# Kernel tuning notes

Measured on AMD Instinct MI355X. Metric: run time of the kernel, lower is better.

Reference implementation:

```python
import jax, jax.numpy as jnp
import numpy as np

B, L, HID = 2, 2048, 1024
H, D = 16, 64            # num_attention_heads, attention_head_size
R = 512                  # projection_rank = basis_rank
MAX_ORDER = 5
NUM_BASIS = MAX_ORDER + 1  # min(basis_rank, max_order+1)
TOPK = 64


def _orthogonal_basis(seq_len, num_basis, dtype=jnp.float32):
    # Orthonormal DCT-II basis evaluated at relative distance d=|i-j|.
    # basis[i, j, k] = s_k * cos(pi * (d + 0.5) * k / L), s_0=sqrt(1/L), s_k=sqrt(2/L)
    idx = jnp.arange(seq_len)
    d = jnp.abs(idx[:, None] - idx[None, :]).astype(dtype)          # [L, L]
    k = jnp.arange(num_basis, dtype=dtype)                          # [K]
    basis = jnp.cos(jnp.pi * (d[..., None] + 0.5) * k / seq_len)    # [L, L, K]
    scale = jnp.where(k == 0, jnp.sqrt(1.0 / seq_len), jnp.sqrt(2.0 / seq_len))
    return basis * scale


def _topk_mask(seq_len, topk):
    # keep top-k nearest neighbors by |i-j| per row (stable argsort tie-break)
    idx = jnp.arange(seq_len)
    dist = jnp.abs(idx[:, None] - idx[None, :])
    k = min(topk, seq_len)
    cols = jnp.argsort(dist, axis=-1)[:, :k]                        # [L, k]
    rows = jnp.broadcast_to(idx[:, None], (seq_len, k))
    mask = jnp.zeros((seq_len, seq_len), dtype=bool).at[rows, cols].set(True)
    return mask


def setup_inputs() -> dict:
    key = jax.random.key(0)
    ks = jax.random.split(key, 10)
    s = 0.02
    inp = {
        "hidden_states": jax.random.normal(ks[0], (B, L, HID), jnp.float32),
        "Wq": jax.random.normal(ks[1], (HID, HID), jnp.float32) * s,
        "bq": jnp.zeros((HID,), jnp.float32),
        "Wk": jax.random.normal(ks[2], (HID, HID), jnp.float32) * s,
        "bk": jnp.zeros((HID,), jnp.float32),
        "Wv": jax.random.normal(ks[3], (HID, HID), jnp.float32) * s,
        "bv": jnp.zeros((HID,), jnp.float32),
        "coefficients": jax.random.normal(ks[4], (H, NUM_BASIS), jnp.float32) * s,
    }
    # orthogonal-ish init for the low-rank projections [H, D, R]
    def ortho(k):
        m = jax.random.normal(k, (H * D, R), jnp.float32)
        q, _ = jnp.linalg.qr(m)
        return q.reshape(H, D, R)
    inp["q_proj_weight"] = ortho(ks[5])
    inp["k_proj_weight"] = ortho(ks[6])
    return inp


def reference(hidden_states, Wq, bq, Wk, bk, Wv, bv, coefficients,
              q_proj_weight, k_proj_weight):
    bsz, tgt_len, _ = hidden_states.shape

    def shape(x):  # [B, L, HID] -> [B, H, L, D]
        return x.reshape(bsz, tgt_len, H, D).transpose(0, 2, 1, 3)

    q = shape(hidden_states @ Wq + bq)
    k = shape(hidden_states @ Wk + bk)
    v = shape(hidden_states @ Wv + bv)

    qp = jnp.einsum('bhld,hdr->bhlr', q, q_proj_weight)
    kp = jnp.einsum('bhld,hdr->bhlr', k, k_proj_weight)
    scores = jnp.einsum('bhlr,bhmr->bhlm', qp, kp) / jnp.sqrt(jnp.float32(R))

    basis = _orthogonal_basis(tgt_len, NUM_BASIS, scores.dtype)      # [L, L, K]
    bias = jnp.einsum('hk,ijk->hij', coefficients, basis)            # [H, L, L]
    bias = bias * _topk_mask(tgt_len, TOPK)[None, :, :]
    scores = scores + bias[None]

    probs = jax.nn.softmax(scores, axis=-1)                          # dropout: eval mode
    ctx = jnp.einsum('bhlm,bhmd->bhld', probs, v)
    return ctx.transpose(0, 2, 1, 3).reshape(bsz, tgt_len, H * D)
```

## Files before the change

kernel.cpp:

```cpp
#include <hip/hip_runtime.h>

typedef short bf16x8 __attribute__((ext_vector_type(8)));
typedef float f32x4 __attribute__((ext_vector_type(4)));

#define L_SEQ 2048

__device__ inline unsigned short f2bf(float f) {
    unsigned int u = __builtin_bit_cast(unsigned int, f);
    u += 0x7FFFu + ((u >> 16) & 1u);
    return (unsigned short)(u >> 16);
}

__device__ inline float exp2_fast(float x) {
    float r;
    asm volatile("v_exp_f32 %0, %1" : "=v"(r) : "v"(x));
    return r;
}

__device__ inline void gload16(const void* g, void* l) {
    __builtin_amdgcn_global_load_lds((const __attribute__((address_space(1))) void*)g,
                                     (__attribute__((address_space(3))) void*)l, 16, 0, 0);
}

__global__ __launch_bounds__(256) void compute_M(const float* __restrict__ Pq,
                                                 const float* __restrict__ Pk,
                                                 float* __restrict__ M) {
    const int h = blockIdx.x, dg = blockIdx.y, t = threadIdx.x;
    const int e = t & 63, dr = t >> 6;
    __shared__ float Pql[4][512];
    for (int i = t; i < 512; i += 256) {
#pragma unroll
        for (int rr = 0; rr < 4; ++rr)
            Pql[rr][i] = Pq[((size_t)h * 64 + dg * 4 + rr) * 512 + i];
    }
    __syncthreads();
    const float4* a = (const float4*)Pql[dr];
    const float4* b = (const float4*)(Pk + ((size_t)h * 64 + e) * 512);
    float s = 0.f;
#pragma unroll 4
    for (int r = 0; r < 128; ++r) {
        float4 x = a[r], y = b[r];
        s = fmaf(x.x, y.x, fmaf(x.y, y.y, fmaf(x.z, y.z, fmaf(x.w, y.w, s))));
    }
    M[((size_t)h * 64 + dg * 4 + dr) * 64 + e] =
        s * (0.044194173824159216f * 1.4426950408889634f);
}

__global__ void bias_table_kernel(const float* __restrict__ coef, float* __restrict__ fbias) {
    int i = blockIdx.x * 256 + threadIdx.x;
    if (i >= 16 * 2048) return;
    int h = i >> 11, d = i & 2047;
    const float pi = 3.14159265358979323846f;
    float acc = 0.f;
#pragma unroll
    for (int k = 0; k < 6; ++k) {
        float sc = (k == 0) ? 0.022097086912079608f : 0.03125f;
        float arg = pi * ((float)d + 0.5f) * (float)k * (1.0f / 2048.0f);
        acc += coef[h * 6 + k] * sc * cosf(arg);
    }
    fbias[i] = acc * 1.4426950408889634f;
}

__global__ __launch_bounds__(256) void build_wtq(
    const float* __restrict__ Wq, const float* __restrict__ bq, const float* __restrict__ M,
    unsigned short* __restrict__ Wt, float* __restrict__ biasp) {
    const int hh = blockIdx.x, kt = blockIdx.y, t = threadIdx.x;
    const int k0 = kt * 64;
    __shared__ float Wql[64 * 68];
    __shared__ float MlT[64 * 65];

    for (int i = t; i < 4096; i += 256) {
        int d = i >> 6, e = i & 63;
        MlT[e * 65 + d] = M[(size_t)hh * 4096 + i];
    }
#pragma unroll
    for (int i = 0; i < 4; ++i) {
        int cc = i * 256 + t;
        int row = cc >> 4, c4 = cc & 15;
        *(float4*)&Wql[row * 68 + c4 * 4] =
            *(const float4*)(Wq + (size_t)(k0 + row) * 1024 + hh * 64 + c4 * 4);
    }
    __syncthreads();

    const int e = t >> 2, kq = t & 3;
    float me[64];
#pragma unroll
    for (int d = 0; d < 64; ++d) me[d] = MlT[e * 65 + d];

    float acc[16];
#pragma unroll
    for (int i = 0; i < 16; ++i) acc[i] = 0.f;
#pragma unroll
    for (int kk = 0; kk < 16; ++kk) {
        int row = kq * 16 + kk;
#pragma unroll
        for (int d4 = 0; d4 < 16; ++d4) {
            float4 w = *(const float4*)&Wql[row * 68 + d4 * 4];
            acc[kk] = fmaf(w.x, me[d4 * 4 + 0],
                      fmaf(w.y, me[d4 * 4 + 1],
                      fmaf(w.z, me[d4 * 4 + 2],
                      fmaf(w.w, me[d4 * 4 + 3], acc[kk]))));
        }
    }
    unsigned short* dp = Wt + (size_t)(hh * 64 + e) * 1024 + k0 + kq * 16;
#pragma unroll
    for (int q8 = 0; q8 < 2; ++q8) {
        unsigned short o8[8];
#pragma unroll
        for (int j = 0; j < 8; ++j) o8[j] = f2bf(acc[q8 * 8 + j]);
        *(uint4*)(dp + q8 * 8) = *(const uint4*)o8;
    }
    if (kt == 0 && t < 64) {
        float s = 0.f;
#pragma unroll
        for (int d = 0; d < 64; ++d) s = fmaf(bq[hh * 64 + d], MlT[t * 65 + d], s);
        biasp[hh * 64 + t] = s;
    }
}

__global__ __launch_bounds__(256) void transpose_wkv(
    const float* __restrict__ Wk, const float* __restrict__ Wv,
    const float* __restrict__ bk, const float* __restrict__ bv,
    unsigned short* __restrict__ Wt, float* __restrict__ biasp) {
    const int ct = blockIdx.x, kt2 = blockIdx.y, sel = blockIdx.z;
    const float* W = sel ? Wv : Wk;
    __shared__ float tl[64 * 68];
    const int t = threadIdx.x;
    const int k0 = kt2 * 64, c0 = ct * 64;
#pragma unroll
    for (int i = 0; i < 4; ++i) {
        int cc = i * 256 + t;
        int r = cc >> 4, c4 = cc & 15;
        *(float4*)&tl[r * 68 + c4 * 4] =
            *(const float4*)(W + (size_t)(k0 + r) * 1024 + c0 + c4 * 4);
    }
    __syncthreads();
    const int c = t >> 2, seg = t & 3;
    unsigned short* dp = Wt + (size_t)(1024 + sel * 1024 + c0 + c) * 1024 + k0 + seg * 16;
#pragma unroll
    for (int q8 = 0; q8 < 2; ++q8) {
        unsigned short o8[8];
#pragma unroll
        for (int j = 0; j < 8; ++j) o8[j] = f2bf(tl[(seg * 16 + q8 * 8 + j) * 68 + c]);
        *(uint4*)(dp + q8 * 8) = *(const uint4*)o8;
    }
    if (kt2 == 0 && t < 64) biasp[1024 + sel * 1024 + c0 + t] = (sel ? bv : bk)[c0 + t];
}

__global__ __launch_bounds__(256) void cast_hs_kernel(const float* __restrict__ hs,
                                                      unsigned short* __restrict__ X) {
    const int i = (blockIdx.x * 256 + threadIdx.x) * 4;
    float4 v = *(const float4*)(hs + i);
    unsigned short o[4] = {f2bf(v.x), f2bf(v.y), f2bf(v.z), f2bf(v.w)};
    *(uint2*)(X + i) = *(const uint2*)o;
}

__global__ __launch_bounds__(512) void gemm_qkv(
    const unsigned short* __restrict__ X, const unsigned short* __restrict__ Wt,
    const float* __restrict__ biasp,
    unsigned short* __restrict__ qs, unsigned short* __restrict__ ksd,
    unsigned short* __restrict__ vt) {
    __shared__ __align__(16) unsigned short shm[4 * 8192];

    const int bn = blockIdx.x, bm = blockIdx.y;
    const int m0 = bm * 128, n0 = bn * 128;
    const int t = threadIdx.x, wave = t >> 6, lane = t & 63, g = lane >> 4, li = lane & 15;
    const int wr = wave >> 2, wc = wave & 3;

    const int rowb = t >> 3;
    const int soff = ((t & 7) ^ (rowb & 7)) * 8;
    const unsigned short* Xrow = X + (size_t)(m0 + rowb) * 1024 + soff;
    const unsigned short* Wrow = Wt + (size_t)(n0 + rowb) * 1024 + soff;

    f32x4 acc[4][2];
#pragma unroll
    for (int i = 0; i < 4; ++i)
#pragma unroll
        for (int j = 0; j < 2; ++j) acc[i][j] = (f32x4){0.f, 0.f, 0.f, 0.f};

#pragma unroll
    for (int i = 0; i < 2; ++i) {
        gload16(Xrow + (size_t)i * 64 * 1024, &shm[(i * 512 + t) * 8]);
        gload16(Wrow + (size_t)i * 64 * 1024, &shm[16384 + (i * 512 + t) * 8]);
    }

    for (int kt = 0; kt < 16; ++kt) {
        const int cur = kt & 1;
        __builtin_amdgcn_s_barrier();
        if (kt < 15) {
            const int k0n = (kt + 1) * 64;
            unsigned short* An = &shm[(cur ^ 1) * 8192];
            unsigned short* Bn = &shm[16384 + (cur ^ 1) * 8192];
#pragma unroll
            for (int i = 0; i < 2; ++i) {
                gload16(Xrow + (size_t)i * 64 * 1024 + k0n, &An[(i * 512 + t) * 8]);
                gload16(Wrow + (size_t)i * 64 * 1024 + k0n, &Bn[(i * 512 + t) * 8]);
            }
            asm volatile("s_waitcnt vmcnt(4)" ::: "memory");
        } else {
            asm volatile("s_waitcnt vmcnt(0)" ::: "memory");
        }
        __builtin_amdgcn_s_barrier();
        const unsigned short* Al = &shm[cur * 8192];
        const unsigned short* Bl = &shm[16384 + cur * 8192];
        __builtin_amdgcn_s_setprio(1);
#pragma unroll
        for (int ks = 0; ks < 2; ++ks) {
            bf16x8 af[4], bf[2];
#pragma unroll
            for (int mi = 0; mi < 4; ++mi) {
                int row = wr * 64 + mi * 16 + li;
                af[mi] = *(const bf16x8*)&Al[row * 64 + ((ks * 4 + g) ^ (row & 7)) * 8];
            }
#pragma unroll
            for (int ni = 0; ni < 2; ++ni) {
                int row = wc * 32 + ni * 16 + li;
                bf[ni] = *(const bf16x8*)&Bl[row * 64 + ((ks * 4 + g) ^ (row & 7)) * 8];
            }
#pragma unroll
            for (int mi = 0; mi < 4; ++mi)
#pragma unroll
                for (int ni = 0; ni < 2; ++ni)
                    acc[mi][ni] = __builtin_amdgcn_mfma_f32_16x16x32_bf16(af[mi], bf[ni],
                                                                          acc[mi][ni], 0, 0, 0);
        }
        __builtin_amdgcn_s_setprio(0);
    }
    __syncthreads();

    float bvals[2];
#pragma unroll
    for (int ni = 0; ni < 2; ++ni) bvals[ni] = biasp[n0 + wc * 32 + ni * 16 + li];

    const int region = n0 >> 10;
    float* scr = (float*)shm;

    if (region < 2) {
        float* wf = scr + wave * (16 * 36);
        unsigned short* dstbase = region == 0 ? qs : ksd;
        const int ncol0 = n0 + wc * 32;
        const int hh = (ncol0 & 1023) >> 6;
        const int dcol = (ncol0 & 63) + (lane & 3) * 8;
        const int lr = lane >> 2;
#pragma unroll
        for (int mi = 0; mi < 4; ++mi) {
#pragma unroll
            for (int r = 0; r < 4; ++r) {
                int rowl = g * 4 + r;
#pragma unroll
                for (int ni = 0; ni < 2; ++ni)
                    wf[rowl * 36 + ni * 16 + li] = acc[mi][ni][r] + bvals[ni];
            }
            int m = m0 + wr * 64 + mi * 16 + lr;
            int bb = m >> 11, l = m & 2047;
            unsigned short* dp = dstbase + ((size_t)(bb * 16 + hh) * 2048 + l) * 64 + dcol;
            float4 a0 = *(const float4*)&wf[lr * 36 + (lane & 3) * 8];
            float4 a1 = *(const float4*)&wf[lr * 36 + (lane & 3) * 8 + 4];
            unsigned short o8[8] = {f2bf(a0.x), f2bf(a0.y), f2bf(a0.z), f2bf(a0.w),
                                    f2bf(a1.x), f2bf(a1.y), f2bf(a1.z), f2bf(a1.w)};
            *(uint4*)dp = *(const uint4*)o8;
        }
    } else {
        float* wf = scr + wave * (32 * 36);
        const int d32 = lane & 31, half = lane >> 5;
        const int dglob = ((n0 + wc * 32) & 63) + d32;
        const int hh = ((n0 + wc * 32) & 1023) >> 6;
#pragma unroll
        for (int ch2 = 0; ch2 < 2; ++ch2) {
#pragma unroll
            for (int mi2 = 0; mi2 < 2; ++mi2) {
                int mi = ch2 * 2 + mi2;
#pragma unroll
                for (int r = 0; r < 4; ++r) {
                    int rowl = mi2 * 16 + g * 4 + r;
#pragma unroll
                    for (int ni = 0; ni < 2; ++ni)
                        wf[rowl * 36 + ni * 16 + li] = acc[mi][ni][r] + bvals[ni];
                }
            }
            int l0 = m0 + wr * 64 + ch2 * 32;
            int bb = l0 >> 11, lb = (l0 & 2047) + half * 16;
            unsigned short* dp = vt + ((size_t)(bb * 16 + hh) * 64 + dglob) * 2048 + lb;
#pragma unroll
            for (int q8 = 0; q8 < 2; ++q8) {
                unsigned short o8[8];
#pragma unroll
                for (int j = 0; j < 8; ++j)
                    o8[j] = f2bf(wf[(half * 16 + q8 * 8 + j) * 36 + d32]);
                *(uint4*)(dp + q8 * 8) = *(const uint4*)o8;
            }
        }
    }
}

__global__ __launch_bounds__(512) void attn_kernel(
    const unsigned short* __restrict__ qs, const unsigned short* __restrict__ ksrc,
    const unsigned short* __restrict__ vt, const float* __restrict__ fbias,
    float* __restrict__ out) {
    const int qt = blockIdx.x, bh = blockIdx.y;
    const int h = bh & 15, b = bh >> 4;
    const int t = threadIdx.x, wave = t >> 6, lane = t & 63, g = lane >> 4, li = lane & 15;

    __shared__ unsigned short Klds[2][2][64 * 64];
    __shared__ unsigned short Vlds[2][2][64 * 64];
    __shared__ unsigned short Plds[8][16 * 64];

    const float* fbh = fbias + (size_t)h * 2048;
    const unsigned short* Kg = ksrc + (size_t)bh * L_SEQ * 64;
    const unsigned short* Vg = vt + (size_t)bh * 64 * L_SEQ;

    const int im = qt * 128 + wave * 16;
    const unsigned short* qb = qs + ((size_t)bh * L_SEQ + im + li) * 64;
    bf16x8 qa0 = *(const bf16x8*)(qb + g * 8);
    bf16x8 qa1 = *(const bf16x8*)(qb + 32 + g * 8);

    bf16x8 onesv;
#pragma unroll
    for (int i = 0; i < 8; ++i) onesv[i] = (short)0x3F80;

    f32x4 o[5];
#pragma unroll
    for (int i = 0; i < 5; ++i) o[i] = (f32x4){0.f, 0.f, 0.f, 0.f};

    const int iout0 = im + g * 4;

    int lo_min = im - 32; lo_min = lo_min < 0 ? 0 : (lo_min > 1984 ? 1984 : lo_min);
    int hi_tmp = im + 15 - 32; hi_tmp = hi_tmp < 0 ? 0 : (hi_tmp > 1984 ? 1984 : hi_tmp);
    const int hi_max = hi_tmp + 63;

    const int r0 = t >> 3, s0 = ((t & 7) ^ (r0 & 7)) * 8;

#pragma unroll
    for (int sub = 0; sub < 2; ++sub) {
        gload16(Kg + (size_t)(sub * 64 + r0) * 64 + s0, &Klds[0][sub][t * 8]);
        gload16(Vg + (size_t)r0 * L_SEQ + sub * 64 + s0, &Vlds[0][sub][t * 8]);
    }

    for (int jp = 0; jp < 16; ++jp) {
        const int cur = jp & 1;

        __builtin_amdgcn_s_barrier();
        if (jp < 15) {
            const int jb = (jp + 1) * 128;
#pragma unroll
            for (int sub = 0; sub < 2; ++sub) {
                gload16(Kg + (size_t)(jb + sub * 64 + r0) * 64 + s0, &Klds[cur ^ 1][sub][t * 8]);
                gload16(Vg + (size_t)r0 * L_SEQ + jb + sub * 64 + s0, &Vlds[cur ^ 1][sub][t * 8]);
            }
            asm volatile("s_waitcnt vmcnt(4)" ::: "memory");
        } else {
            asm volatile("s_waitcnt vmcnt(0)" ::: "memory");
        }
        __builtin_amdgcn_s_barrier();

#pragma unroll
        for (int sub = 0; sub < 2; ++sub) {
            const int j0 = jp * 128 + sub * 64;
            const unsigned short* Kl = Klds[cur][sub];
            const unsigned short* Vl = Vlds[cur][sub];

            f32x4 s[4];
#pragma unroll
            for (int nb = 0; nb < 4; ++nb) s[nb] = (f32x4){0.f, 0.f, 0.f, 0.f};
            __builtin_amdgcn_s_setprio(1);
#pragma unroll
            for (int ks = 0; ks < 2; ++ks) {
                bf16x8 qf = ks ? qa1 : qa0;
#pragma unroll
                for (int nb = 0; nb < 4; ++nb) {
                    int row = nb * 16 + li;
                    bf16x8 kf = *(const bf16x8*)&Kl[row * 64 + ((ks * 4 + g) ^ (row & 7)) * 8];
                    s[nb] = __builtin_amdgcn_mfma_f32_16x16x32_bf16(qf, kf, s[nb], 0, 0, 0);
                }
            }
            __builtin_amdgcn_s_setprio(0);

            const bool bias_tile = (j0 + 63 >= lo_min) && (j0 <= hi_max);
            unsigned short* Pw = Plds[wave];
#pragma unroll
            for (int r = 0; r < 4; ++r) {
                int iout = iout0 + r;
                int row = g * 4 + r;
                if (bias_tile) {
                    int lo = iout - 32;
                    lo = lo < 0 ? 0 : (lo > 1984 ? 1984 : lo);
#pragma unroll
                    for (int nb = 0; nb < 4; ++nb) {
                        int j = j0 + nb * 16 + li;
                        float x = s[nb][r];
                        int dd = iout - j; dd = dd < 0 ? -dd : dd;
                        if ((unsigned)(j - lo) < 64u) x += fbh[dd];
                        int col = nb * 16 + li;
                        Pw[row * 64 + (col ^ ((row & 7) << 3))] = f2bf(exp2_fast(x));
                    }
                } else {
#pragma unroll
                    for (int nb = 0; nb < 4; ++nb) {
                        int col = nb * 16 + li;
                        Pw[row * 64 + (col ^ ((row & 7) << 3))] = f2bf(exp2_fast(s[nb][r]));
                    }
                }
            }

            bf16x8 pa0 = *(const bf16x8*)&Pw[li * 64 + ((0 + g) ^ (li & 7)) * 8];
            bf16x8 pa1 = *(const bf16x8*)&Pw[li * 64 + ((4 + g) ^ (li & 7)) * 8];
            __builtin_amdgcn_s_setprio(1);
#pragma unroll
            for (int db = 0; db < 4; ++db) {
                int row = db * 16 + li;
                bf16x8 v0 = *(const bf16x8*)&Vl[row * 64 + ((0 + g) ^ (row & 7)) * 8];
                bf16x8 v1 = *(const bf16x8*)&Vl[row * 64 + ((4 + g) ^ (row & 7)) * 8];
                o[db] = __builtin_amdgcn_mfma_f32_16x16x32_bf16(pa0, v0, o[db], 0, 0, 0);
                o[db] = __builtin_amdgcn_mfma_f32_16x16x32_bf16(pa1, v1, o[db], 0, 0, 0);
            }
            o[4] = __builtin_amdgcn_mfma_f32_16x16x32_bf16(pa0, onesv, o[4], 0, 0, 0);
            o[4] = __builtin_amdgcn_mfma_f32_16x16x32_bf16(pa1, onesv, o[4], 0, 0, 0);
            __builtin_amdgcn_s_setprio(0);
        }
    }

    float* ob = out + (size_t)b * L_SEQ * 1024 + h * 64;
#pragma unroll
    for (int r = 0; r < 4; ++r) {
        float rl = 1.f / o[4][r];
        int iout = iout0 + r;
#pragma unroll
        for (int db = 0; db < 4; ++db)
            ob[(size_t)iout * 1024 + db * 16 + li] = o[db][r] * rl;
    }
}

extern "C" void kernel_launch(void* const* d_in, const int* in_sizes, int n_in,
                              void* d_out, int out_size, void* d_ws, size_t ws_size,
                              hipStream_t stream) {
    const float* hs = (const float*)d_in[0];
    const float* Wq = (const float*)d_in[1];
    const float* bq = (const float*)d_in[2];
    const float* Wk = (const float*)d_in[3];
    const float* bk = (const float*)d_in[4];
    const float* Wv = (const float*)d_in[5];
    const float* bv = (const float*)d_in[6];
    const float* coef = (const float*)d_in[7];
    const float* Pq = (const float*)d_in[8];
    const float* Pk = (const float*)d_in[9];
    float* out = (float*)d_out;

    char* w = (char*)d_ws;
    float* M = (float*)(w);
    float* fbias = (float*)(w + 0x40000);
    float* biasp = (float*)(w + 0x60000);
    unsigned short* Wt = (unsigned short*)(w + 0x70000);
    unsigned short* X = (unsigned short*)(w + 0x670000);
    unsigned short* qs = (unsigned short*)(w + 0xE70000);
    unsigned short* ks = (unsigned short*)(w + 0x1670000);
    unsigned short* vt = (unsigned short*)(w + 0x2670000);

    hipLaunchKernelGGL(compute_M, dim3(16, 16), dim3(256), 0, stream, Pq, Pk, M);
    hipLaunchKernelGGL(bias_table_kernel, dim3(128), dim3(256), 0, stream, coef, fbias);
    hipLaunchKernelGGL(build_wtq, dim3(16, 16), dim3(256), 0, stream, Wq, bq, M, Wt, biasp);
    hipLaunchKernelGGL(transpose_wkv, dim3(16, 16, 2), dim3(256), 0, stream,
                       Wk, Wv, bk, bv, Wt, biasp);
    hipLaunchKernelGGL(cast_hs_kernel, dim3(4096), dim3(256), 0, stream, hs, X);
    hipLaunchKernelGGL(gemm_qkv, dim3(24, 32), dim3(512), 0, stream, X, Wt, biasp, qs, ks, vt);
    hipLaunchKernelGGL(attn_kernel, dim3(16, 32), dim3(512), 0, stream, qs, ks, vt, fbias, out);
}
```

Before: 124.2 us.

## Process two 16-row query tiles per wave to reuse K/V fragments

```diff
diff --git a/kernel.cpp b/kernel.cpp
--- a/kernel.cpp
+++ b/kernel.cpp
@@ -303,29 +303,35 @@
 
     __shared__ unsigned short Klds[2][2][64 * 64];
     __shared__ unsigned short Vlds[2][2][64 * 64];
-    __shared__ unsigned short Plds[8][16 * 64];
+    __shared__ unsigned short Plds[8][32 * 64];
 
     const float* fbh = fbias + (size_t)h * 2048;
     const unsigned short* Kg = ksrc + (size_t)bh * L_SEQ * 64;
     const unsigned short* Vg = vt + (size_t)bh * 64 * L_SEQ;
 
-    const int im = qt * 128 + wave * 16;
+    const int im = qt * 256 + wave * 32;
     const unsigned short* qb = qs + ((size_t)bh * L_SEQ + im + li) * 64;
-    bf16x8 qa0 = *(const bf16x8*)(qb + g * 8);
-    bf16x8 qa1 = *(const bf16x8*)(qb + 32 + g * 8);
+    bf16x8 qa00 = *(const bf16x8*)(qb + g * 8);
+    bf16x8 qa01 = *(const bf16x8*)(qb + 32 + g * 8);
+    bf16x8 qa10 = *(const bf16x8*)(qb + 16 * 64 + g * 8);
+    bf16x8 qa11 = *(const bf16x8*)(qb + 16 * 64 + 32 + g * 8);
 
     bf16x8 onesv;
 #pragma unroll
     for (int i = 0; i < 8; ++i) onesv[i] = (short)0x3F80;
 
-    f32x4 o[5];
-#pragma unroll
-    for (int i = 0; i < 5; ++i) o[i] = (f32x4){0.f, 0.f, 0.f, 0.f};
-
-    const int iout0 = im + g * 4;
+    f32x4 oA[5], oB[5];
+#pragma unroll
+    for (int i = 0; i < 5; ++i) {
+        oA[i] = (f32x4){0.f, 0.f, 0.f, 0.f};
+        oB[i] = (f32x4){0.f, 0.f, 0.f, 0.f};
+    }
+
+    const int ioutA = im + g * 4;
+    const int ioutB = im + 16 + g * 4;
 
     int lo_min = im - 32; lo_min = lo_min < 0 ? 0 : (lo_min > 1984 ? 1984 : lo_min);
-    int hi_tmp = im + 15 - 32; hi_tmp = hi_tmp < 0 ? 0 : (hi_tmp > 1984 ? 1984 : hi_tmp);
+    int hi_tmp = im + 31 - 32; hi_tmp = hi_tmp < 0 ? 0 : (hi_tmp > 1984 ? 1984 : hi_tmp);
     const int hi_max = hi_tmp + 63;
 
     const int r0 = t >> 3, s0 = ((t & 7) ^ (r0 & 7)) * 8;
@@ -359,27 +365,39 @@
             const unsigned short* Kl = Klds[cur][sub];
             const unsigned short* Vl = Vlds[cur][sub];
 
-            f32x4 s[4];
-#pragma unroll
-            for (int nb = 0; nb < 4; ++nb) s[nb] = (f32x4){0.f, 0.f, 0.f, 0.f};
+            bf16x8 kf0[4], kf1[4];
+#pragma unroll
+            for (int nb = 0; nb < 4; ++nb) {
+                int row = nb * 16 + li;
+                kf0[nb] = *(const bf16x8*)&Kl[row * 64 + ((0 + g) ^ (row & 7)) * 8];
+                kf1[nb] = *(const bf16x8*)&Kl[row * 64 + ((4 + g) ^ (row & 7)) * 8];
+            }
+
+            f32x4 sA[4], sB[4];
+#pragma unroll
+            for (int nb = 0; nb < 4; ++nb) {
+                sA[nb] = (f32x4){0.f, 0.f, 0.f, 0.f};
+                sB[nb] = (f32x4){0.f, 0.f, 0.f, 0.f};
+            }
             __builtin_amdgcn_s_setprio(1);
 #pragma unroll
-            for (int ks = 0; ks < 2; ++ks) {
-                bf16x8 qf = ks ? qa1 : qa0;
-#pragma unroll
-                for (int nb = 0; nb < 4; ++nb) {
-                    int row = nb * 16 + li;
-                    bf16x8 kf = *(const bf16x8*)&Kl[row * 64 + ((ks * 4 + g) ^ (row & 7)) * 8];
-                    s[nb] = __builtin_amdgcn_mfma_f32_16x16x32_bf16(qf, kf, s[nb], 0, 0, 0);
-                }
+            for (int nb = 0; nb < 4; ++nb) {
+                sA[nb] = __builtin_amdgcn_mfma_f32_16x16x32_bf16(qa00, kf0[nb], sA[nb], 0, 0, 0);
+                sA[nb] = __builtin_amdgcn_mfma_f32_16x16x32_bf16(qa01, kf1[nb], sA[nb], 0, 0, 0);
+            }
+#pragma unroll
+            for (int nb = 0; nb < 4; ++nb) {
+                sB[nb] = __builtin_amdgcn_mfma_f32_16x16x32_bf16(qa10, kf0[nb], sB[nb], 0, 0, 0);
+                sB[nb] = __builtin_amdgcn_mfma_f32_16x16x32_bf16(qa11, kf1[nb], sB[nb], 0, 0, 0);
             }
             __builtin_amdgcn_s_setprio(0);
 
             const bool bias_tile = (j0 + 63 >= lo_min) && (j0 <= hi_max);
             unsigned short* Pw = Plds[wave];
+
 #pragma unroll
             for (int r = 0; r < 4; ++r) {
-                int iout = iout0 + r;
+                int iout = ioutA + r;
                 int row = g * 4 + r;
                 if (bias_tile) {
                     int lo = iout - 32;
@@ -387,7 +405,7 @@
 #pragma unroll
                     for (int nb = 0; nb < 4; ++nb) {
                         int j = j0 + nb * 16 + li;
-                        float x = s[nb][r];
+                        float x = sA[nb][r];
                         int dd = iout - j; dd = dd < 0 ? -dd : dd;
                         if ((unsigned)(j - lo) < 64u) x += fbh[dd];
                         int col = nb * 16 + li;
@@ -397,24 +415,63 @@
 #pragma unroll
                     for (int nb = 0; nb < 4; ++nb) {
                         int col = nb * 16 + li;
-                        Pw[row * 64 + (col ^ ((row & 7) << 3))] = f2bf(exp2_fast(s[nb][r]));
+                        Pw[row * 64 + (col ^ ((row & 7) << 3))] = f2bf(exp2_fast(sA[nb][r]));
                     }
                 }
             }
-
-            bf16x8 pa0 = *(const bf16x8*)&Pw[li * 64 + ((0 + g) ^ (li & 7)) * 8];
-            bf16x8 pa1 = *(const bf16x8*)&Pw[li * 64 + ((4 + g) ^ (li & 7)) * 8];
-            __builtin_amdgcn_s_setprio(1);
+#pragma unroll
+            for (int r = 0; r < 4; ++r) {
+                int iout = ioutB + r;
+                int row = 16 + g * 4 + r;
+                if (bias_tile) {
+                    int lo = iout - 32;
+                    lo = lo < 0 ? 0 : (lo > 1984 ? 1984 : lo);
+#pragma unroll
+                    for (int nb = 0; nb < 4; ++nb) {
+                        int j = j0 + nb * 16 + li;
+                        float x = sB[nb][r];
+                        int dd = iout - j; dd = dd < 0 ? -dd : dd;
+                        if ((unsigned)(j - lo) < 64u) x += fbh[dd];
+                        int col = nb * 16 + li;
+                        Pw[row * 64 + (col ^ ((row & 7) << 3))] = f2bf(exp2_fast(x));
+                    }
+                } else {
+#pragma unroll
+                    for (int nb = 0; nb < 4; ++nb) {
+                        int col = nb * 16 + li;
+                        Pw[row * 64 + (col ^ ((row & 7) << 3))] = f2bf(exp2_fast(sB[nb][r]));
+                    }
+                }
+            }
+
+            bf16x8 paA0 = *(const bf16x8*)&Pw[li * 64 + ((0 + g) ^ (li & 7)) * 8];
+            bf16x8 paA1 = *(const bf16x8*)&Pw[li * 64 + ((4 + g) ^ (li & 7)) * 8];
+            bf16x8 paB0 = *(const bf16x8*)&Pw[(16 + li) * 64 + ((0 + g) ^ ((16 + li) & 7)) * 8];
+            bf16x8 paB1 = *(const bf16x8*)&Pw[(16 + li) * 64 + ((4 + g) ^ ((16 + li) & 7)) * 8];
+
+            bf16x8 vf0[4], vf1[4];
 #pragma unroll
             for (int db = 0; db < 4; ++db) {
                 int row = db * 16 + li;
-                bf16x8 v0 = *(const bf16x8*)&Vl[row * 64 + ((0 + g) ^ (row & 7)) * 8];
-                bf16x8 v1 = *(const bf16x8*)&Vl[row * 64 + ((4 + g) ^ (row & 7)) * 8];
-                o[db] = __builtin_amdgcn_mfma_f32_16x16x32_bf16(pa0, v0, o[db], 0, 0, 0);
-                o[db] = __builtin_amdgcn_mfma_f32_16x16x32_bf16(pa1, v1, o[db], 0, 0, 0);
-            }
-            o[4] = __builtin_amdgcn_mfma_f32_16x16x32_bf16(pa0, onesv, o[4], 0, 0, 0);
-            o[4] = __builtin_amdgcn_mfma_f32_16x16x32_bf16(pa1, onesv, o[4], 0, 0, 0);
+                vf0[db] = *(const bf16x8*)&Vl[row * 64 + ((0 + g) ^ (row & 7)) * 8];
+                vf1[db] = *(const bf16x8*)&Vl[row * 64 + ((4 + g) ^ (row & 7)) * 8];
+            }
+
+            __builtin_amdgcn_s_setprio(1);
+#pragma unroll
+            for (int db = 0; db < 4; ++db) {
+                oA[db] = __builtin_amdgcn_mfma_f32_16x16x32_bf16(paA0, vf0[db], oA[db], 0, 0, 0);
+                oA[db] = __builtin_amdgcn_mfma_f32_16x16x32_bf16(paA1, vf1[db], oA[db], 0, 0, 0);
+            }
+            oA[4] = __builtin_amdgcn_mfma_f32_16x16x32_bf16(paA0, onesv, oA[4], 0, 0, 0);
+            oA[4] = __builtin_amdgcn_mfma_f32_16x16x32_bf16(paA1, onesv, oA[4], 0, 0, 0);
+#pragma unroll
+            for (int db = 0; db < 4; ++db) {
+                oB[db] = __builtin_amdgcn_mfma_f32_16x16x32_bf16(paB0, vf0[db], oB[db], 0, 0, 0);
+                oB[db] = __builtin_amdgcn_mfma_f32_16x16x32_bf16(paB1, vf1[db], oB[db], 0, 0, 0);
+            }
+            oB[4] = __builtin_amdgcn_mfma_f32_16x16x32_bf16(paB0, onesv, oB[4], 0, 0, 0);
+            oB[4] = __builtin_amdgcn_mfma_f32_16x16x32_bf16(paB1, onesv, oB[4], 0, 0, 0);
             __builtin_amdgcn_s_setprio(0);
         }
     }
@@ -422,11 +479,14 @@
     float* ob = out + (size_t)b * L_SEQ * 1024 + h * 64;
 #pragma unroll
     for (int r = 0; r < 4; ++r) {
-        float rl = 1.f / o[4][r];
-        int iout = iout0 + r;
-#pragma unroll
-        for (int db = 0; db < 4; ++db)
-            ob[(size_t)iout * 1024 + db * 16 + li] = o[db][r] * rl;
+        float rlA = 1.f / oA[4][r];
+        float rlB = 1.f / oB[4][r];
+        int ia = ioutA + r, ib = ioutB + r;
+#pragma unroll
+        for (int db = 0; db < 4; ++db) {
+            ob[(size_t)ia * 1024 + db * 16 + li] = oA[db][r] * rlA;
+            ob[(size_t)ib * 1024 + db * 16 + li] = oB[db][r] * rlB;
+        }
     }
 }
 
@@ -462,5 +522,5 @@
                        Wk, Wv, bk, bv, Wt, biasp);
     hipLaunchKernelGGL(cast_hs_kernel, dim3(4096), dim3(256), 0, stream, hs, X);
     hipLaunchKernelGGL(gemm_qkv, dim3(24, 32), dim3(512), 0, stream, X, Wt, biasp, qs, ks, vt);
-    hipLaunchKernelGGL(attn_kernel, dim3(16, 32), dim3(512), 0, stream, qs, ks, vt, fbias, out);
-}
+    hipLaunchKernelGGL(attn_kernel, dim3(8, 32), dim3(512), 0, stream, qs, ks, vt, fbias, out);
+}
```

Measured after the change: 137.7 us. 10.9% more time.

## Transpose MFMA operands in attention loop and compute softmax denominator via shuffles

Applied to the files above, without the earlier changes.

```diff
diff --git a/kernel.cpp b/kernel.cpp
--- a/kernel.cpp
+++ b/kernel.cpp
@@ -314,19 +314,19 @@
     bf16x8 qa0 = *(const bf16x8*)(qb + g * 8);
     bf16x8 qa1 = *(const bf16x8*)(qb + 32 + g * 8);
 
-    bf16x8 onesv;
-#pragma unroll
-    for (int i = 0; i < 8; ++i) onesv[i] = (short)0x3F80;
-
-    f32x4 o[5];
-#pragma unroll
-    for (int i = 0; i < 5; ++i) o[i] = (f32x4){0.f, 0.f, 0.f, 0.f};
-
-    const int iout0 = im + g * 4;
+    f32x4 o[4];
+#pragma unroll
+    for (int i = 0; i < 4; ++i) o[i] = (f32x4){0.f, 0.f, 0.f, 0.f};
+    float denacc = 0.f;
+
+    const int iout = im + li;
+    int lo = iout - 32; lo = lo < 0 ? 0 : (lo > 1984 ? 1984 : lo);
 
     int lo_min = im - 32; lo_min = lo_min < 0 ? 0 : (lo_min > 1984 ? 1984 : lo_min);
     int hi_tmp = im + 15 - 32; hi_tmp = hi_tmp < 0 ? 0 : (hi_tmp > 1984 ? 1984 : hi_tmp);
     const int hi_max = hi_tmp + 63;
+
+    const int swz = (li & 7) << 1;
 
     const int r0 = t >> 3, s0 = ((t & 7) ^ (r0 & 7)) * 8;
 
@@ -370,63 +370,62 @@
                 for (int nb = 0; nb < 4; ++nb) {
                     int row = nb * 16 + li;
                     bf16x8 kf = *(const bf16x8*)&Kl[row * 64 + ((ks * 4 + g) ^ (row & 7)) * 8];
-                    s[nb] = __builtin_amdgcn_mfma_f32_16x16x32_bf16(qf, kf, s[nb], 0, 0, 0);
+                    s[nb] = __builtin_amdgcn_mfma_f32_16x16x32_bf16(kf, qf, s[nb], 0, 0, 0);
                 }
             }
             __builtin_amdgcn_s_setprio(0);
 
             const bool bias_tile = (j0 + 63 >= lo_min) && (j0 <= hi_max);
             unsigned short* Pw = Plds[wave];
-#pragma unroll
-            for (int r = 0; r < 4; ++r) {
-                int iout = iout0 + r;
-                int row = g * 4 + r;
-                if (bias_tile) {
-                    int lo = iout - 32;
-                    lo = lo < 0 ? 0 : (lo > 1984 ? 1984 : lo);
-#pragma unroll
-                    for (int nb = 0; nb < 4; ++nb) {
-                        int j = j0 + nb * 16 + li;
-                        float x = s[nb][r];
+            float den = 0.f;
+#pragma unroll
+            for (int nb = 0; nb < 4; ++nb) {
+                unsigned int uu[4];
+#pragma unroll
+                for (int r = 0; r < 4; ++r) {
+                    int j = j0 + nb * 16 + g * 4 + r;
+                    float x = s[nb][r];
+                    if (bias_tile) {
                         int dd = iout - j; dd = dd < 0 ? -dd : dd;
                         if ((unsigned)(j - lo) < 64u) x += fbh[dd];
-                        int col = nb * 16 + li;
-                        Pw[row * 64 + (col ^ ((row & 7) << 3))] = f2bf(exp2_fast(x));
                     }
-                } else {
-#pragma unroll
-                    for (int nb = 0; nb < 4; ++nb) {
-                        int col = nb * 16 + li;
-                        Pw[row * 64 + (col ^ ((row & 7) << 3))] = f2bf(exp2_fast(s[nb][r]));
-                    }
+                    unsigned int u = (unsigned int)f2bf(exp2_fast(x));
+                    den += __builtin_bit_cast(float, u << 16);
+                    uu[r] = u;
                 }
-            }
-
-            bf16x8 pa0 = *(const bf16x8*)&Pw[li * 64 + ((0 + g) ^ (li & 7)) * 8];
-            bf16x8 pa1 = *(const bf16x8*)&Pw[li * 64 + ((4 + g) ^ (li & 7)) * 8];
+                int cs = (nb * 4 + g) ^ swz;
+                uint2 pw2;
+                pw2.x = uu[0] | (uu[1] << 16);
+                pw2.y = uu[2] | (uu[3] << 16);
+                *(uint2*)&Pw[li * 64 + cs * 4] = pw2;
+            }
+            den += __shfl_xor(den, 16);
+            den += __shfl_xor(den, 32);
+            denacc += den;
+
+            bf16x8 pb0 = *(const bf16x8*)&Pw[li * 64 + ((g * 2) ^ swz) * 4];
+            bf16x8 pb1 = *(const bf16x8*)&Pw[li * 64 + ((8 + g * 2) ^ swz) * 4];
+
             __builtin_amdgcn_s_setprio(1);
 #pragma unroll
             for (int db = 0; db < 4; ++db) {
                 int row = db * 16 + li;
                 bf16x8 v0 = *(const bf16x8*)&Vl[row * 64 + ((0 + g) ^ (row & 7)) * 8];
                 bf16x8 v1 = *(const bf16x8*)&Vl[row * 64 + ((4 + g) ^ (row & 7)) * 8];
-                o[db] = __builtin_amdgcn_mfma_f32_16x16x32_bf16(pa0, v0, o[db], 0, 0, 0);
-                o[db] = __builtin_amdgcn_mfma_f32_16x16x32_bf16(pa1, v1, o[db], 0, 0, 0);
-            }
-            o[4] = __builtin_amdgcn_mfma_f32_16x16x32_bf16(pa0, onesv, o[4], 0, 0, 0);
-            o[4] = __builtin_amdgcn_mfma_f32_16x16x32_bf16(pa1, onesv, o[4], 0, 0, 0);
+                o[db] = __builtin_amdgcn_mfma_f32_16x16x32_bf16(v0, pb0, o[db], 0, 0, 0);
+                o[db] = __builtin_amdgcn_mfma_f32_16x16x32_bf16(v1, pb1, o[db], 0, 0, 0);
+            }
             __builtin_amdgcn_s_setprio(0);
         }
     }
 
-    float* ob = out + (size_t)b * L_SEQ * 1024 + h * 64;
-#pragma unroll
-    for (int r = 0; r < 4; ++r) {
-        float rl = 1.f / o[4][r];
-        int iout = iout0 + r;
-#pragma unroll
-        for (int db = 0; db < 4; ++db)
-            ob[(size_t)iout * 1024 + db * 16 + li] = o[db][r] * rl;
+    float rl = 1.f / denacc;
+    float* ob2 = out + ((size_t)b * L_SEQ + iout) * 1024 + h * 64;
+#pragma unroll
+    for (int db = 0; db < 4; ++db) {
+        f32x4 vsc = o[db];
+        vsc[0] *= rl; vsc[1] *= rl; vsc[2] *= rl; vsc[3] *= rl;
+        *(f32x4*)(ob2 + db * 16 + g * 4) = vsc;
     }
 }
 
```

After: 130.0 us. +4.7%, slower.
